# Kernel optimization log

Hardware: AMD Instinct MI355X
Metric: run time of the kernel (lower is better)

## Reference

```python
import jax, jax.numpy as jnp
import numpy as np

B, T, S, M = 512, 256, 32, 4  # groups, timesteps, state dim, measure dim


def setup_inputs() -> dict:
    key = jax.random.key(0)
    k = jax.random.split(key, 7)
    obs = jax.random.normal(k[0], (B, T, M), jnp.float32)
    # stable transition matrix: scaled orthogonal
    A = jax.random.normal(k[1], (S, S), jnp.float32)
    F = (0.95 * jnp.linalg.qr(A)[0]).astype(jnp.float32)
    # PSD process noise
    Aq = jax.random.normal(k[2], (S, S), jnp.float32)
    Q = (0.05 * (Aq @ Aq.T) / S + 0.01 * jnp.eye(S)).astype(jnp.float32)
    H = (jax.random.normal(k[3], (M, S), jnp.float32) / jnp.sqrt(S)).astype(jnp.float32)
    # PSD measurement noise
    Ar = jax.random.normal(k[4], (M, M), jnp.float32)
    R = ((Ar @ Ar.T) / M + 0.1 * jnp.eye(M)).astype(jnp.float32)
    init_mean = jax.random.normal(k[5], (B, S), jnp.float32)
    Ai = jax.random.normal(k[6], (B, S, S), jnp.float32)
    init_cov = (jnp.einsum('bij,bkj->bik', Ai, Ai) / S + 0.1 * jnp.eye(S)).astype(jnp.float32)
    return {'input': obs, 'F': F, 'Q': Q, 'H': H, 'R': R,
            'init_mean': init_mean, 'init_cov': init_cov}


def reference(input, F, Q, H, R, init_mean, init_cov):
    """One-step-ahead Kalman filter predictions.
    Returns (meas_means [T,B,M], meas_covs [T,B,M,M])."""

    def step(carry, y):
        m, P = carry  # m: [B,S], P: [B,S,S]
        # --- update with observation y (time t-1) ---
        PHt = jnp.einsum('bij,mj->bim', P, H)                    # [B,S,M]
        Smeas = jnp.einsum('ms,bsn->bmn', H, PHt) + R            # [B,M,M]
        # K = P H^T S^{-1}  (S symmetric)
        K = jnp.swapaxes(jnp.linalg.solve(Smeas, jnp.swapaxes(PHt, -1, -2)), -1, -2)  # [B,S,M]
        resid = y - m @ H.T                                      # [B,M]
        m_u = m + jnp.einsum('bsm,bm->bs', K, resid)
        # (I - K H) P ; note H P = PHt^T since P symmetric
        P_u = P - jnp.einsum('bsm,bim->bsi', K, PHt)
        # --- predict ---
        m_p = m_u @ F.T
        P_p = jnp.einsum('ij,bjk,lk->bil', F, P_u, F) + Q
        # --- measurement distribution ---
        mm = m_p @ H.T                                           # [B,M]
        mc = jnp.einsum('ms,bsi,ni->bmn', H, P_p, H) + R         # [B,M,M]
        return (m_p, P_p), (mm, mc)

    # t = 0: measurement of the initial state prediction
    mm0 = init_mean @ H.T
    mc0 = jnp.einsum('ms,bsi,ni->bmn', H, init_cov, H) + R
    obs_tm1 = jnp.swapaxes(input[:, :-1, :], 0, 1)               # [T-1,B,M]
    _, (mms, mcs) = jax.lax.scan(step, (init_mean, init_cov), obs_tm1)
    meas_means = jnp.concatenate([mm0[None], mms], axis=0)       # [T,B,M]
    meas_covs = jnp.concatenate([mc0[None], mcs], axis=0)        # [T,B,M,M]
    return meas_means, meas_covs
```

## Files before the change

kernel.cpp:

```cpp
#include <hip/hip_runtime.h>

#define BB 512
#define TT 256
#define PS 40

typedef __attribute__((ext_vector_type(2)))  _Float16 h2;
typedef __attribute__((ext_vector_type(4)))  _Float16 h4;
typedef __attribute__((ext_vector_type(8)))  _Float16 h8;
typedef __attribute__((ext_vector_type(4)))  unsigned u4v;
typedef __attribute__((ext_vector_type(16))) float f16v;
typedef __attribute__((ext_vector_type(4)))  float f4v;

#define MFMA(a,b,c) __builtin_amdgcn_mfma_f32_32x32x16_f16((a),(b),(c),0,0,0)

static __device__ __forceinline__ void pksplit(float x0, float x1, unsigned& hi, unsigned& lo) {
    h2 h = __builtin_bit_cast(h2, __builtin_amdgcn_cvt_pkrtz(x0, x1));
    h2 l = __builtin_bit_cast(h2, __builtin_amdgcn_cvt_pkrtz(x0 - (float)h[0], x1 - (float)h[1]));
    hi = __builtin_bit_cast(unsigned, h);
    lo = __builtin_bit_cast(unsigned, l);
}

static __device__ __forceinline__ void mkfrag(const f16v M, int h, h8 Ah[2], h8 Al[2]) {
    unsigned ph[8], pl[8], xh[8], xl[8];
    #pragma unroll
    for (int q = 0; q < 8; ++q) pksplit(M[2*q], M[2*q+1], ph[q], pl[q]);
    #pragma unroll
    for (int q = 0; q < 8; ++q) {
        xh[q] = (unsigned)__shfl_xor((int)ph[q], 32, 64);
        xl[q] = (unsigned)__shfl_xor((int)pl[q], 32, 64);
    }
    u4v a0h = { h ? xh[2] : ph[0], h ? xh[3] : ph[1], h ? ph[2] : xh[0], h ? ph[3] : xh[1] };
    u4v a1h = { h ? xh[6] : ph[4], h ? xh[7] : ph[5], h ? ph[6] : xh[4], h ? ph[7] : xh[5] };
    u4v a0l = { h ? xl[2] : pl[0], h ? xl[3] : pl[1], h ? pl[2] : xl[0], h ? pl[3] : xl[1] };
    u4v a1l = { h ? xl[6] : pl[4], h ? xl[7] : pl[5], h ? pl[6] : xl[4], h ? pl[7] : xl[5] };
    Ah[0] = __builtin_bit_cast(h8, a0h);  Ah[1] = __builtin_bit_cast(h8, a1h);
    Al[0] = __builtin_bit_cast(h8, a0l);  Al[1] = __builtin_bit_cast(h8, a1l);
}

static __device__ __forceinline__ h8 ld8h(const _Float16* p) {
    h4 a = *(const h4*)p;
    h4 b = *(const h4*)(p + 4);
    h8 r;
    r[0]=a[0]; r[1]=a[1]; r[2]=a[2]; r[3]=a[3];
    r[4]=b[0]; r[5]=b[1]; r[6]=b[2]; r[7]=b[3];
    return r;
}

__global__ __launch_bounds__(64, 1)
void kalman_v7(const float* __restrict__ obs,
               const float* __restrict__ Fg,
               const float* __restrict__ Qg,
               const float* __restrict__ Hg,
               const float* __restrict__ Rg,
               const float* __restrict__ im,
               const float* __restrict__ ic,
               float* __restrict__ out)
{
    __shared__ __align__(16) _Float16 sPNh[4*PS], sPNl[4*PS];
    __shared__ __align__(16) float sm[32];
    __shared__ __align__(16) float sS[16];
    __shared__ __align__(16) float sRes4[4];

    const int lane = threadIdx.x;
    const int b    = blockIdx.x;
    const int c    = lane & 31;
    const int h    = lane >> 5;

    h8 Fh[2], Fl[2], Hh[2], Hl[2];
    #pragma unroll
    for (int kk = 0; kk < 2; ++kk) {
        #pragma unroll
        for (int j = 0; j < 8; ++j) {
            int k = kk*16 + h*8 + j;
            float f = Fg[c*32 + k];
            _Float16 fh = (_Float16)f;
            Fh[kk][j] = fh;
            Fl[kk][j] = (_Float16)(f - (float)fh);
            float hv = (c < 4) ? Hg[c*32 + k] : 0.f;
            _Float16 hh = (_Float16)hv;
            Hh[kk][j] = hh;
            Hl[kk][j] = (_Float16)(hv - (float)hh);
        }
    }

    float Frow[32];
    #pragma unroll
    for (int k = 0; k < 32; ++k)
        Frow[k] = (lane < 32) ? Fg[c*32 + k] : Hg[(lane & 3)*32 + k];

    f16v Qc, P;
    #pragma unroll
    for (int reg = 0; reg < 16; ++reg) {
        int row = (reg & 3) + 8*(reg >> 2) + 4*h;
        Qc[reg] = Qg[row*32 + c];
        P[reg]  = ic[(size_t)b*1024 + row*32 + c];
    }
    float Rc[4] = {0.f, 0.f, 0.f, 0.f};
    if (c < 4) {
        #pragma unroll
        for (int m = 0; m < 4; ++m) Rc[m] = Rg[m*4 + c];
    }
    if (lane < 32) sm[lane] = im[b*32 + lane];

    const bool yl = (lane >= 32 && lane < 36);
    const float* obsp = obs + (size_t)b*TT*4 + (yl ? (lane - 32) : 0);
    float* om = out;
    float* oc = out + (size_t)TT * BB * 4;

    float yv = yl ? obsp[0] : 0.f;

    for (int t = 0; t < TT; ++t) {
        float yv_nxt = (yl && t + 1 < TT) ? obsp[(t + 1) * 4] : 0.f;

        float dotv = 0.f;
        #pragma unroll
        for (int q = 0; q < 8; ++q) {
            f4v mv = *(const f4v*)&sm[4*q];
            dotv += Frow[4*q+0]*mv.x + Frow[4*q+1]*mv.y
                  + Frow[4*q+2]*mv.z + Frow[4*q+3]*mv.w;
        }

        h8 Ph[2], Pl[2];
        mkfrag(P, h, Ph, Pl);

        f16v aA = 0.0f, aB = 0.0f;
        aA = MFMA(Hh[0], Ph[0], aA);  aB = MFMA(Hh[1], Ph[1], aB);
        aA = MFMA(Hh[0], Pl[0], aA);  aB = MFMA(Hh[1], Pl[1], aB);
        aA = MFMA(Hl[0], Ph[0], aA);  aB = MFMA(Hl[1], Ph[1], aB);

        if (lane < 32) {
            unsigned h01, l01, h23, l23;
            pksplit(aA[0]+aB[0], aA[1]+aB[1], h01, l01);
            pksplit(aA[2]+aB[2], aA[3]+aB[3], h23, l23);
            h2 H01 = __builtin_bit_cast(h2, h01), L01 = __builtin_bit_cast(h2, l01);
            h2 H23 = __builtin_bit_cast(h2, h23), L23 = __builtin_bit_cast(h2, l23);
            sPNh[0*PS + c] = H01[0];  sPNh[1*PS + c] = H01[1];
            sPNh[2*PS + c] = H23[0];  sPNh[3*PS + c] = H23[1];
            sPNl[0*PS + c] = L01[0];  sPNl[1*PS + c] = L01[1];
            sPNl[2*PS + c] = L23[0];  sPNl[3*PS + c] = L23[1];
        }

        f16v tA = 0.0f, tB = 0.0f;
        tA = MFMA(Ph[0], Fh[0], tA);  tB = MFMA(Ph[1], Fh[1], tB);
        tA = MFMA(Ph[0], Fl[0], tA);  tB = MFMA(Ph[1], Fl[1], tB);
        tA = MFMA(Pl[0], Fh[0], tA);  tB = MFMA(Pl[1], Fh[1], tB);

        h8 N0h, N1h, N0l, N1l;
        if (c < 4) {
            N0h = ld8h(&sPNh[c*PS + 8*h]);
            N1h = ld8h(&sPNh[c*PS + 16 + 8*h]);
            N0l = ld8h(&sPNl[c*PS + 8*h]);
            N1l = ld8h(&sPNl[c*PS + 16 + 8*h]);
        } else {
            N0h = (h8)(_Float16)0; N1h = (h8)(_Float16)0;
            N0l = (h8)(_Float16)0; N1l = (h8)(_Float16)0;
        }

        f16v sA = 0.0f, sB = 0.0f;
        sA = MFMA(Hh[0], N0h, sA);  sB = MFMA(Hh[1], N1h, sB);
        sA = MFMA(Hh[0], N0l, sA);  sB = MFMA(Hh[1], N1l, sB);
        sA = MFMA(Hl[0], N0h, sA);  sB = MFMA(Hl[1], N1h, sB);

        f16v wA = 0.0f, wB = 0.0f;
        wA = MFMA(N0h, Fh[0], wA);  wB = MFMA(N1h, Fh[1], wB);
        wA = MFMA(N0h, Fl[0], wA);  wB = MFMA(N1h, Fl[1], wB);
        wA = MFMA(N0l, Fh[0], wA);  wB = MFMA(N1l, Fh[1], wB);

        f16v Tp = tA + tB;
        h8 Th[2], Tl[2];
        mkfrag(Tp, h, Th, Tl);

        f16v zA = Qc, zB = 0.0f;
        zA = MFMA(Fh[0], Th[0], zA);  zB = MFMA(Fh[1], Th[1], zB);
        zA = MFMA(Fh[0], Tl[0], zA);  zB = MFMA(Fh[1], Tl[1], zB);
        zA = MFMA(Fl[0], Th[0], zA);  zB = MFMA(Fl[1], Th[1], zB);

        float Smr[4];
        #pragma unroll
        for (int m = 0; m < 4; ++m) Smr[m] = sA[m] + sB[m] + Rc[m];
        if (lane < 32 && c < 4) {
            #pragma unroll
            for (int m = 0; m < 4; ++m)
                oc[(((size_t)t*BB + b)*4 + m)*4 + c] = Smr[m];
            *(f4v*)&sS[c*4] = (f4v){Smr[0], Smr[1], Smr[2], Smr[3]};
        }
        if (yl) {
            om[((size_t)t*BB + b)*4 + (lane - 32)] = dotv;
            sRes4[lane - 32] = yv - dotv;
        }

        if (t == TT - 1) break;
        yv = yv_nxt;

        f4v q0 = *(const f4v*)&sS[0];
        f4v q1 = *(const f4v*)&sS[4];
        f4v q2 = *(const f4v*)&sS[8];
        f4v q3 = *(const f4v*)&sS[12];
        const float S0=q0.x,  S1=q1.x,  S2=q2.x,  S3=q3.x;
        const float S4=q0.y,  S5=q1.y,  S6=q2.y,  S7=q3.y;
        const float S8=q0.z,  S9=q1.z,  S10=q2.z, S11=q3.z;
        const float S12=q0.w, S13=q1.w, S14=q2.w, S15=q3.w;

        float nG0, nG1, nG2, nG3, W0, W1, W2, W3;
        {
            const float A2323 = S10*S15 - S11*S14;
            const float A1323 = S9 *S15 - S11*S13;
            const float A1223 = S9 *S14 - S10*S13;
            const float A0323 = S8 *S15 - S11*S12;
            const float A0223 = S8 *S14 - S10*S12;
            const float A0123 = S8 *S13 - S9 *S12;
            const float A2313 = S6 *S15 - S7 *S14;
            const float A1313 = S5 *S15 - S7 *S13;
            const float A1213 = S5 *S14 - S6 *S13;
            const float A2312 = S6 *S11 - S7 *S10;
            const float A1312 = S5 *S11 - S7 *S9;
            const float A1212 = S5 *S10 - S6 *S9;
            const float A0313 = S4 *S15 - S7 *S12;
            const float A0213 = S4 *S14 - S6 *S12;
            const float A0312 = S4 *S11 - S7 *S8;
            const float A0212 = S4 *S10 - S6 *S8;
            const float A0113 = S4 *S13 - S5 *S12;
            const float A0112 = S4 *S9  - S5 *S8;

            const float i00 =  (S5*A2323 - S6*A1323 + S7*A1223);
            const float i10 = -(S4*A2323 - S6*A0323 + S7*A0223);
            const float i20 =  (S4*A1323 - S5*A0323 + S7*A0123);
            const float i30 = -(S4*A1223 - S5*A0223 + S6*A0123);
            const float i01 = -(S1*A2323 - S2*A1323 + S3*A1223);
            const float i11 =  (S0*A2323 - S2*A0323 + S3*A0223);
            const float i21 = -(S0*A1323 - S1*A0323 + S3*A0123);
            const float i31 =  (S0*A1223 - S1*A0223 + S2*A0123);
            const float i02 =  (S1*A2313 - S2*A1313 + S3*A1213);
            const float i12 = -(S0*A2313 - S2*A0313 + S3*A0213);
            const float i22 =  (S0*A1313 - S1*A0313 + S3*A0113);
            const float i32 = -(S0*A1213 - S1*A0213 + S2*A0113);
            const float i03 = -(S1*A2312 - S2*A1312 + S3*A1212);
            const float i13 =  (S0*A2312 - S2*A0312 + S3*A0212);
            const float i23 = -(S0*A1312 - S1*A0312 + S3*A0112);
            const float i33 =  (S0*A1212 - S1*A0212 + S2*A0112);

            const float det = S0*i00 + S1*i10 + S2*i20 + S3*i30;
            const float nid = -1.0f / det;

            W0 = wA[0] + wB[0];
            W1 = wA[1] + wB[1];
            W2 = wA[2] + wB[2];
            W3 = wA[3] + wB[3];

            nG0 = nid * (W0*i00 + W1*i10 + W2*i20 + W3*i30);
            nG1 = nid * (W0*i01 + W1*i11 + W2*i21 + W3*i31);
            nG2 = nid * (W0*i02 + W1*i12 + W2*i22 + W3*i32);
            nG3 = nid * (W0*i03 + W1*i13 + W2*i23 + W3*i33);
        }

        h8 Gh8, Gl8, Wh8, Wl8;
        {
            unsigned g01, gl01, g23, gl23, w01, wl01, w23, wl23;
            pksplit(nG0, nG1, g01, gl01);
            pksplit(nG2, nG3, g23, gl23);
            pksplit(W0, W1, w01, wl01);
            pksplit(W2, W3, w23, wl23);
            u4v gh = {g01, g23, 0u, 0u}, gl = {gl01, gl23, 0u, 0u};
            u4v wh = {w01, w23, 0u, 0u}, wl = {wl01, wl23, 0u, 0u};
            Gh8 = __builtin_bit_cast(h8, gh);  Gl8 = __builtin_bit_cast(h8, gl);
            Wh8 = __builtin_bit_cast(h8, wh);  Wl8 = __builtin_bit_cast(h8, wl);
        }
        zA = MFMA(Gh8, Wh8, zA);
        zB = MFMA(Gh8, Wl8, zB);
        zA = MFMA(Gl8, Wh8, zA);
        P = zA + zB;

        {
            f4v rv = *(const f4v*)&sRes4[0];
            if (lane < 32)
                sm[lane] = dotv - (nG0*rv.x + nG1*rv.y + nG2*rv.z + nG3*rv.w);
        }
    }
}

extern "C" void kernel_launch(void* const* d_in, const int* in_sizes, int n_in,
                              void* d_out, int out_size, void* d_ws, size_t ws_size,
                              hipStream_t stream) {
    const float* obs       = (const float*)d_in[0];
    const float* F         = (const float*)d_in[1];
    const float* Q         = (const float*)d_in[2];
    const float* H         = (const float*)d_in[3];
    const float* R         = (const float*)d_in[4];
    const float* init_mean = (const float*)d_in[5];
    const float* init_cov  = (const float*)d_in[6];
    float* out = (float*)d_out;

    kalman_v7<<<BB, 64, 0, stream>>>(obs, F, Q, H, R, init_mean, init_cov, out);
}
```

Measured before the change: 563.3 us.

## Shorten per-step dependency chain: derive W from T, shuffle S, split accumulators

Reworks the per-timestep recurrence. W is now computed as H·T from the existing P·F product instead of from a separate LDS round-trip of P·Hᵀ. The staged PHᵀ values are stored only as the fp16 high part, which drops the low-part compensation terms for S. The innovation covariance and the residuals now move between lanes with register shuffles instead of shared memory. MFMA accumulations are split into independent chains so the matrix unit can overlap them. The goal is to cut the serial latency per step and the LDS traffic, at the cost of some accuracy in S.

```diff
diff --git a/kernel.cpp b/kernel.cpp
--- a/kernel.cpp
+++ b/kernel.cpp
@@ -13,9 +13,12 @@
 
 #define MFMA(a,b,c) __builtin_amdgcn_mfma_f32_32x32x16_f16((a),(b),(c),0,0,0)
 
+static __device__ __forceinline__ h2 pkh2(float x0, float x1) {
+    return __builtin_bit_cast(h2, __builtin_amdgcn_cvt_pkrtz(x0, x1));
+}
 static __device__ __forceinline__ void pksplit(float x0, float x1, unsigned& hi, unsigned& lo) {
-    h2 h = __builtin_bit_cast(h2, __builtin_amdgcn_cvt_pkrtz(x0, x1));
-    h2 l = __builtin_bit_cast(h2, __builtin_amdgcn_cvt_pkrtz(x0 - (float)h[0], x1 - (float)h[1]));
+    h2 h = pkh2(x0, x1);
+    h2 l = pkh2(x0 - (float)h[0], x1 - (float)h[1]);
     hi = __builtin_bit_cast(unsigned, h);
     lo = __builtin_bit_cast(unsigned, l);
 }
@@ -47,7 +50,7 @@
 }
 
 __global__ __launch_bounds__(64, 1)
-void kalman_v7(const float* __restrict__ obs,
+void kalman_v9(const float* __restrict__ obs,
                const float* __restrict__ Fg,
                const float* __restrict__ Qg,
                const float* __restrict__ Hg,
@@ -56,10 +59,8 @@
                const float* __restrict__ ic,
                float* __restrict__ out)
 {
-    __shared__ __align__(16) _Float16 sPNh[4*PS], sPNl[4*PS];
+    __shared__ __align__(16) _Float16 sPN[4*PS];
     __shared__ __align__(16) float sm[32];
-    __shared__ __align__(16) float sS[16];
-    __shared__ __align__(16) float sRes4[4];
 
     const int lane = threadIdx.x;
     const int b    = blockIdx.x;
@@ -123,85 +124,87 @@
         h8 Ph[2], Pl[2];
         mkfrag(P, h, Ph, Pl);
 
-        f16v aA = 0.0f, aB = 0.0f;
-        aA = MFMA(Hh[0], Ph[0], aA);  aB = MFMA(Hh[1], Ph[1], aB);
-        aA = MFMA(Hh[0], Pl[0], aA);  aB = MFMA(Hh[1], Pl[1], aB);
-        aA = MFMA(Hl[0], Ph[0], aA);  aB = MFMA(Hl[1], Ph[1], aB);
+        f16v hp1 = MFMA(Hh[0], Ph[0], (f16v)0.0f);
+        f16v hp2 = MFMA(Hl[0], Ph[0], (f16v)0.0f);
+        hp1 = MFMA(Hh[1], Ph[1], hp1);
+        hp2 = MFMA(Hl[1], Ph[1], hp2);
+
+        f16v u1 = MFMA(Ph[0], Fh[0], (f16v)0.0f);
+        f16v u2 = MFMA(Ph[0], Fl[0], (f16v)0.0f);
+        f16v u3 = MFMA(Pl[0], Fh[0], (f16v)0.0f);
+        u1 = MFMA(Ph[1], Fh[1], u1);
+        u2 = MFMA(Ph[1], Fl[1], u2);
+        u3 = MFMA(Pl[1], Fh[1], u3);
+
+        float residv = yv - dotv;
+        yv = yv_nxt;
+        if (yl) om[((size_t)t*BB + b)*4 + (lane - 32)] = dotv;
+        float r0 = __shfl(residv, 32, 64), r1 = __shfl(residv, 33, 64);
+        float r2 = __shfl(residv, 34, 64), r3 = __shfl(residv, 35, 64);
 
         if (lane < 32) {
-            unsigned h01, l01, h23, l23;
-            pksplit(aA[0]+aB[0], aA[1]+aB[1], h01, l01);
-            pksplit(aA[2]+aB[2], aA[3]+aB[3], h23, l23);
-            h2 H01 = __builtin_bit_cast(h2, h01), L01 = __builtin_bit_cast(h2, l01);
-            h2 H23 = __builtin_bit_cast(h2, h23), L23 = __builtin_bit_cast(h2, l23);
-            sPNh[0*PS + c] = H01[0];  sPNh[1*PS + c] = H01[1];
-            sPNh[2*PS + c] = H23[0];  sPNh[3*PS + c] = H23[1];
-            sPNl[0*PS + c] = L01[0];  sPNl[1*PS + c] = L01[1];
-            sPNl[2*PS + c] = L23[0];  sPNl[3*PS + c] = L23[1];
-        }
-
-        f16v tA = 0.0f, tB = 0.0f;
-        tA = MFMA(Ph[0], Fh[0], tA);  tB = MFMA(Ph[1], Fh[1], tB);
-        tA = MFMA(Ph[0], Fl[0], tA);  tB = MFMA(Ph[1], Fl[1], tB);
-        tA = MFMA(Pl[0], Fh[0], tA);  tB = MFMA(Pl[1], Fh[1], tB);
-
-        h8 N0h, N1h, N0l, N1l;
-        if (c < 4) {
-            N0h = ld8h(&sPNh[c*PS + 8*h]);
-            N1h = ld8h(&sPNh[c*PS + 16 + 8*h]);
-            N0l = ld8h(&sPNl[c*PS + 8*h]);
-            N1l = ld8h(&sPNl[c*PS + 16 + 8*h]);
-        } else {
-            N0h = (h8)(_Float16)0; N1h = (h8)(_Float16)0;
-            N0l = (h8)(_Float16)0; N1l = (h8)(_Float16)0;
-        }
-
-        f16v sA = 0.0f, sB = 0.0f;
-        sA = MFMA(Hh[0], N0h, sA);  sB = MFMA(Hh[1], N1h, sB);
-        sA = MFMA(Hh[0], N0l, sA);  sB = MFMA(Hh[1], N1l, sB);
-        sA = MFMA(Hl[0], N0h, sA);  sB = MFMA(Hl[1], N1h, sB);
-
-        f16v wA = 0.0f, wB = 0.0f;
-        wA = MFMA(N0h, Fh[0], wA);  wB = MFMA(N1h, Fh[1], wB);
-        wA = MFMA(N0h, Fl[0], wA);  wB = MFMA(N1h, Fl[1], wB);
-        wA = MFMA(N0l, Fh[0], wA);  wB = MFMA(N1l, Fh[1], wB);
-
-        f16v Tp = tA + tB;
+            h2 a01 = pkh2(hp1[0]+hp2[0], hp1[1]+hp2[1]);
+            h2 a23 = pkh2(hp1[2]+hp2[2], hp1[3]+hp2[3]);
+            sPN[0*PS + c] = a01[0];  sPN[1*PS + c] = a01[1];
+            sPN[2*PS + c] = a23[0];  sPN[3*PS + c] = a23[1];
+        }
+
+        f16v Tp = u1 + u2 + u3;
         h8 Th[2], Tl[2];
         mkfrag(Tp, h, Th, Tl);
 
-        f16v zA = Qc, zB = 0.0f;
-        zA = MFMA(Fh[0], Th[0], zA);  zB = MFMA(Fh[1], Th[1], zB);
-        zA = MFMA(Fh[0], Tl[0], zA);  zB = MFMA(Fh[1], Tl[1], zB);
-        zA = MFMA(Fl[0], Th[0], zA);  zB = MFMA(Fl[1], Th[1], zB);
+        h8 N0, N1;
+        if (c < 4) {
+            N0 = ld8h(&sPN[c*PS + 8*h]);
+            N1 = ld8h(&sPN[c*PS + 16 + 8*h]);
+        } else {
+            N0 = (h8)(_Float16)0; N1 = (h8)(_Float16)0;
+        }
+
+        f16v s1 = MFMA(Hh[0], N0, (f16v)0.0f);
+        f16v s2 = MFMA(Hl[0], N0, (f16v)0.0f);
+        s1 = MFMA(Hh[1], N1, s1);
+        s2 = MFMA(Hl[1], N1, s2);
+
+        f16v z1 = MFMA(Fh[0], Th[0], Qc);
+        f16v z2 = MFMA(Fh[0], Tl[0], (f16v)0.0f);
+        f16v z3 = MFMA(Fl[0], Th[0], (f16v)0.0f);
+        f16v w1 = MFMA(Hh[0], Th[0], (f16v)0.0f);
+        f16v w2 = MFMA(Hh[0], Tl[0], (f16v)0.0f);
+        f16v w3 = MFMA(Hl[0], Th[0], (f16v)0.0f);
+        z1 = MFMA(Fh[1], Th[1], z1);
+        z2 = MFMA(Fh[1], Tl[1], z2);
+        z3 = MFMA(Fl[1], Th[1], z3);
+        w1 = MFMA(Hh[1], Th[1], w1);
+        w2 = MFMA(Hh[1], Tl[1], w2);
+        w3 = MFMA(Hl[1], Th[1], w3);
 
         float Smr[4];
         #pragma unroll
-        for (int m = 0; m < 4; ++m) Smr[m] = sA[m] + sB[m] + Rc[m];
-        if (lane < 32 && c < 4) {
+        for (int m = 0; m < 4; ++m) Smr[m] = s1[m] + s2[m] + Rc[m];
+        if (lane < 4) {
             #pragma unroll
             for (int m = 0; m < 4; ++m)
                 oc[(((size_t)t*BB + b)*4 + m)*4 + c] = Smr[m];
-            *(f4v*)&sS[c*4] = (f4v){Smr[0], Smr[1], Smr[2], Smr[3]};
-        }
-        if (yl) {
-            om[((size_t)t*BB + b)*4 + (lane - 32)] = dotv;
-            sRes4[lane - 32] = yv - dotv;
         }
 
         if (t == TT - 1) break;
-        yv = yv_nxt;
-
-        f4v q0 = *(const f4v*)&sS[0];
-        f4v q1 = *(const f4v*)&sS[4];
-        f4v q2 = *(const f4v*)&sS[8];
-        f4v q3 = *(const f4v*)&sS[12];
-        const float S0=q0.x,  S1=q1.x,  S2=q2.x,  S3=q3.x;
-        const float S4=q0.y,  S5=q1.y,  S6=q2.y,  S7=q3.y;
-        const float S8=q0.z,  S9=q1.z,  S10=q2.z, S11=q3.z;
-        const float S12=q0.w, S13=q1.w, S14=q2.w, S15=q3.w;
-
-        float nG0, nG1, nG2, nG3, W0, W1, W2, W3;
+
+        const float S0  = __shfl(Smr[0], 0, 64), S1  = __shfl(Smr[0], 1, 64),
+                    S2  = __shfl(Smr[0], 2, 64), S3  = __shfl(Smr[0], 3, 64);
+        const float S4  = __shfl(Smr[1], 0, 64), S5  = __shfl(Smr[1], 1, 64),
+                    S6  = __shfl(Smr[1], 2, 64), S7  = __shfl(Smr[1], 3, 64);
+        const float S8  = __shfl(Smr[2], 0, 64), S9  = __shfl(Smr[2], 1, 64),
+                    S10 = __shfl(Smr[2], 2, 64), S11 = __shfl(Smr[2], 3, 64);
+        const float S12 = __shfl(Smr[3], 0, 64), S13 = __shfl(Smr[3], 1, 64),
+                    S14 = __shfl(Smr[3], 2, 64), S15 = __shfl(Smr[3], 3, 64);
+
+        const float W0 = w1[0] + w2[0] + w3[0];
+        const float W1 = w1[1] + w2[1] + w3[1];
+        const float W2 = w1[2] + w2[2] + w3[2];
+        const float W3 = w1[3] + w2[3] + w3[3];
+
+        float nG0, nG1, nG2, nG3;
         {
             const float A2323 = S10*S15 - S11*S14;
             const float A1323 = S9 *S15 - S11*S13;
@@ -242,16 +245,14 @@
             const float det = S0*i00 + S1*i10 + S2*i20 + S3*i30;
             const float nid = -1.0f / det;
 
-            W0 = wA[0] + wB[0];
-            W1 = wA[1] + wB[1];
-            W2 = wA[2] + wB[2];
-            W3 = wA[3] + wB[3];
-
             nG0 = nid * (W0*i00 + W1*i10 + W2*i20 + W3*i30);
             nG1 = nid * (W0*i01 + W1*i11 + W2*i21 + W3*i31);
             nG2 = nid * (W0*i02 + W1*i12 + W2*i22 + W3*i32);
             nG3 = nid * (W0*i03 + W1*i13 + W2*i23 + W3*i33);
         }
+
+        if (lane < 32)
+            sm[lane] = dotv - (nG0*r0 + nG1*r1 + nG2*r2 + nG3*r3);
 
         h8 Gh8, Gl8, Wh8, Wl8;
         {
@@ -265,16 +266,11 @@
             Gh8 = __builtin_bit_cast(h8, gh);  Gl8 = __builtin_bit_cast(h8, gl);
             Wh8 = __builtin_bit_cast(h8, wh);  Wl8 = __builtin_bit_cast(h8, wl);
         }
-        zA = MFMA(Gh8, Wh8, zA);
-        zB = MFMA(Gh8, Wl8, zB);
-        zA = MFMA(Gl8, Wh8, zA);
-        P = zA + zB;
-
-        {
-            f4v rv = *(const f4v*)&sRes4[0];
-            if (lane < 32)
-                sm[lane] = dotv - (nG0*rv.x + nG1*rv.y + nG2*rv.z + nG3*rv.w);
-        }
+
+        z1 = MFMA(Gh8, Wh8, z1);
+        z2 = MFMA(Gh8, Wl8, z2);
+        z3 = MFMA(Gl8, Wh8, z3);
+        P = z1 + z2 + z3;
     }
 }
 
@@ -290,5 +286,5 @@
     const float* init_cov  = (const float*)d_in[6];
     float* out = (float*)d_out;
 
-    kalman_v7<<<BB, 64, 0, stream>>>(obs, F, Q, H, R, init_mean, init_cov, out);
-}
+    kalman_v9<<<BB, 64, 0, stream>>>(obs, F, Q, H, R, init_mean, init_cov, out);
+}
```

After: 598.4 us. 1.06x slower.
